# Performance work log

Measured on AMD Instinct MI355X. Metric: run time of the kernel, lower is better.

## Reference

```python
import jax, jax.numpy as jnp
import numpy as np

B = 2
SEQ = 384            # args.seq_len (per-stock sub-sequence length)
N_AUX = 4            # len(args.aux_tickers)
S = SEQ * N_AUX + 1  # global separator token + tiled sub-sequences
D_MODEL = 512
NHEAD = 8
HEAD_DIM = 64
ROPE = 32            # qk_rope_dim
KV_C = 256
Q_C = 384
D_FF = 1536
H2 = NHEAD * 2       # differential attention sub-heads
DH = HEAD_DIM // 2
RH = ROPE // 2
EPS = 1.1920929e-07  # torch RMSNorm default eps (fp32 machine eps)
SCALING = 1.0 / ((HEAD_DIM + ROPE) // 2)
LAMBDA_INIT = 0.8 - 0.6 * float(np.exp(-0.3 * 0))  # depth=0 -> 0.2


def rmsnorm(x, w, eps=EPS):
    return x * jax.lax.rsqrt(jnp.mean(jnp.square(x), -1, keepdims=True) + eps) * w


def apply_rope(xs, cos, sin):
    # xs: [B, N_AUX, SEQ, H2, RH]; cos/sin: [SEQ, RH//2]
    xr = xs[..., 0::2]
    xi = xs[..., 1::2]
    c = cos[None, None, :, None, :]
    s = sin[None, None, :, None, :]
    yr = xr * c - xi * s
    yi = xr * s + xi * c
    return jnp.stack([yr, yi], axis=-1).reshape(xs.shape)


def _build_mask():
    causal = np.triu(np.ones((SEQ, SEQ), np.bool_), 1)
    tiled = np.tile(causal, (N_AUX, N_AUX))
    m = np.ones((S, S), np.bool_)
    m[:, 0] = False          # everyone attends to global separator
    m[1:, 1:] = tiled
    return jnp.asarray(m)[None, None]  # [1,1,S,S], True = masked


MASK = _build_mask()


def setup_inputs() -> dict:
    key = jax.random.key(0)
    ks = jax.random.split(key, 16)

    def w(k, shape, std=0.02):
        return jax.random.normal(k, shape, jnp.float32) * std

    x = jax.random.normal(ks[0], (B, S, D_MODEL), jnp.float32)
    # rope table: complex [SEQ, ROPE//4] stored as (cos, sin)
    pairs = ROPE // 4
    inv = 1.0 / (10000.0 ** (np.arange(pairs, dtype=np.float64) / pairs))
    ang = np.outer(np.arange(SEQ), inv)
    freqs = jnp.asarray(np.stack([np.cos(ang), np.sin(ang)], -1), jnp.float32)
    return {
        'x': x,
        'freqs': freqs,
        'W_kv_down': w(ks[1], (D_MODEL, KV_C + ROPE)),
        'W_q_down': w(ks[2], (D_MODEL, Q_C)),
        'W_kv_up': w(ks[3], (KV_C, NHEAD * HEAD_DIM * 2)),
        'W_q_up': w(ks[4], (Q_C, NHEAD * (HEAD_DIM + ROPE))),
        'kv_norm_w': jnp.ones((KV_C,), jnp.float32),
        'q_norm_w': jnp.ones((Q_C,), jnp.float32),
        'W_o': w(ks[5], (NHEAD * HEAD_DIM, D_MODEL)),
        'lambda_q1': w(ks[6], (DH,), 0.1),
        'lambda_k1': w(ks[7], (DH,), 0.1),
        'lambda_q2': w(ks[8], (DH,), 0.1),
        'lambda_k2': w(ks[9], (DH,), 0.1),
        'head_norm_w': jnp.ones((HEAD_DIM,), jnp.float32),
        'norm1_w': jnp.ones((D_MODEL,), jnp.float32),
        'norm2_w': jnp.ones((D_MODEL,), jnp.float32),
        'W_ff_in': w(ks[10], (D_MODEL, 2 * D_FF)),
        'W_ff_out': w(ks[11], (D_FF, D_MODEL)),
    }


def reference(x, freqs, W_kv_down, W_q_down, W_kv_up, W_q_up, kv_norm_w, q_norm_w,
              W_o, lambda_q1, lambda_k1, lambda_q2, lambda_k2, head_norm_w,
              norm1_w, norm2_w, W_ff_in, W_ff_out):
    cos, sin = freqs[..., 0], freqs[..., 1]
    # ---- attention block (pre-norm) ----
    h = rmsnorm(x, norm1_w)
    ckv_full = h @ W_kv_down                               # [B,S,KV_C+ROPE]
    c_kv, k_rope = ckv_full[..., :KV_C], ckv_full[..., KV_C:]
    kv = (rmsnorm(c_kv, kv_norm_w) @ W_kv_up).reshape(B, S, NHEAD, 2 * HEAD_DIM)
    k, v = kv[..., :HEAD_DIM], kv[..., HEAD_DIM:]
    k = k.reshape(B, S, H2, DH)
    qf = (rmsnorm(h @ W_q_down, q_norm_w) @ W_q_up).reshape(B, S, NHEAD, HEAD_DIM + ROPE)
    q, q_rope = qf[..., :HEAD_DIM], qf[..., HEAD_DIM:]
    q = q.reshape(B, S, H2, DH)
    k_rope = jnp.broadcast_to(k_rope[:, :, None, :], (B, S, NHEAD, ROPE)).reshape(B, S, H2, RH)
    q_rope = q_rope.reshape(B, S, H2, RH)
    # split off global separator token, rope per sub-sequence
    q_sep, q_rot = q_rope[:, :1], q_rope[:, 1:].reshape(B, N_AUX, SEQ, H2, RH)
    k_sep, k_rot = k_rope[:, :1], k_rope[:, 1:].reshape(B, N_AUX, SEQ, H2, RH)
    q_rot = apply_rope(q_rot, cos, sin).reshape(B, S - 1, H2, RH)
    k_rot = apply_rope(k_rot, cos, sin).reshape(B, S - 1, H2, RH)
    q_rope = jnp.concatenate([q_sep, q_rot], axis=1)
    k_rope = jnp.concatenate([k_sep, k_rot], axis=1)
    qh = jnp.concatenate([q, q_rope], -1).transpose(0, 2, 1, 3)  # [B,H2,S,DH+RH]
    kh = jnp.concatenate([k, k_rope], -1).transpose(0, 2, 1, 3)
    a = jnp.einsum('bhqd,bhkd->bhqk', qh, kh) * SCALING
    abs_a = jnp.where(MASK, -1e9, jnp.abs(a))
    p = jnp.sign(a) * jax.nn.softmax(abs_a, axis=-1)
    lam = (jnp.exp(jnp.sum(lambda_q1 * lambda_k1)) -
           jnp.exp(jnp.sum(lambda_q2 * lambda_k2)) + LAMBDA_INIT)
    p = p.reshape(B, NHEAD, 2, S, S)
    G = jnp.mean(p[:, :, 0], axis=-1, keepdims=True)
    att = p[:, :, 0] - lam * p[:, :, 1] + G * lam
    att = jnp.where(MASK, 0.0, att)
    o = jnp.einsum('bhqk,bkhd->bqhd', att, v)              # [B,S,NHEAD,HEAD_DIM]
    o = rmsnorm(o, head_norm_w, 1e-5).reshape(B, S, NHEAD * HEAD_DIM)
    x = x + o @ W_o
    # ---- SwiGLU FFN ----
    h2 = rmsnorm(x, norm2_w)
    uv = h2 @ W_ff_in
    u, g = uv[..., :D_FF], uv[..., D_FF:]
    return x + (u * jax.nn.silu(g)) @ W_ff_out
```

## Files before the change

### kernel.cpp

```cpp
#include <hip/hip_runtime.h>

#define NB 2
#define SEQN 384
#define NS 1537
#define NS_PAD 1600
#define NH 8
#define H2N 16
#define NM (NB*NS)
#define DFF 1536
#define EPS1 1.1920929e-07f
#define SCAL (1.0f/48.0f)
#define SC2 (SCAL * 1.4426950408889634f)

#define SWZ(row, col) ((((row) << 6)) + ((col) ^ (((row) & 7) << 3)))

typedef __bf16 bf16x8 __attribute__((ext_vector_type(8)));
typedef _Float16 f16x8 __attribute__((ext_vector_type(8)));
typedef float f32x4 __attribute__((ext_vector_type(4)));

__device__ __forceinline__ unsigned short f2bf(float f) {
    unsigned int u = __builtin_bit_cast(unsigned int, f);
    u += 0x7FFFu + ((u >> 16) & 1u);
    return (unsigned short)(u >> 16);
}
__device__ __forceinline__ float bf2f(unsigned short h) {
    unsigned int u = ((unsigned int)h) << 16;
    return __builtin_bit_cast(float, u);
}

struct TD { const float* w; unsigned short* hi; unsigned short* lo; int K; int N; int perm; };
struct TD7 { TD d[7]; int tend[7]; };

__global__ __launch_bounds__(256) void transpose_all(TD7 a) {
    __shared__ float tile[32][33];
    int t = blockIdx.x;
    int i = 0;
    while (t >= a.tend[i]) i++;
    int base = (i == 0) ? 0 : a.tend[i - 1];
    int lt = t - base;
    const float* w = a.d[i].w;
    unsigned short* hi = a.d[i].hi;
    unsigned short* lo = a.d[i].lo;
    int K = a.d[i].K, N = a.d[i].N, perm = a.d[i].perm;
    int Nh = N >> 1;
    int kt = (K + 31) / 32;
    int k0 = (lt % kt) * 32, n0 = (lt / kt) * 32;
    int tx = threadIdx.x & 31, ty4 = (threadIdx.x >> 5) * 4;
    for (int q = 0; q < 4; q++) {
        int k = k0 + ty4 + q, n = n0 + tx;
        tile[ty4 + q][tx] = (k < K && n < N) ? w[(size_t)k * N + n] : 0.f;
    }
    __syncthreads();
    for (int q = 0; q < 4; q++) {
        int n = n0 + ty4 + q, k = k0 + tx;
        if (n < N && k < K) {
            float v = tile[tx][ty4 + q];
            unsigned short hb = f2bf(v);
            int n_out = perm ? ((n < Nh) ? 2 * n : 2 * (n - Nh) + 1) : n;
            size_t o = (size_t)n_out * K + k;
            hi[o] = hb;
            if (lo) lo[o] = f2bf(v - bf2f(hb));
        }
    }
}

__global__ __launch_bounds__(256) void rmsnorm_k(const float* __restrict__ in,
    const float* __restrict__ w, unsigned short* __restrict__ hi, unsigned short* __restrict__ lo,
    int in_stride, int C, float eps) {
    int row = blockIdx.x;
    const float* x = in + (size_t)row * in_stride;
    float ss = 0.f;
    for (int j = threadIdx.x; j < C; j += 256) { float v = x[j]; ss += v * v; }
    for (int o = 1; o < 64; o <<= 1) ss += __shfl_xor(ss, o);
    __shared__ float red[4];
    if ((threadIdx.x & 63) == 0) red[threadIdx.x >> 6] = ss;
    __syncthreads();
    ss = red[0] + red[1] + red[2] + red[3];
    float rs = rsqrtf(ss / (float)C + eps);
    for (int j = threadIdx.x; j < C; j += 256) {
        float y = x[j] * rs * w[j];
        unsigned short hb = f2bf(y);
        hi[(size_t)row * C + j] = hb;
        if (lo) lo[(size_t)row * C + j] = f2bf(y - bf2f(hb));
    }
}

__global__ __launch_bounds__(256) void rmsnorm_dual(const float* __restrict__ cq,
    const float* __restrict__ wA, const float* __restrict__ wB,
    unsigned short* __restrict__ ah, unsigned short* __restrict__ al,
    unsigned short* __restrict__ bh_, unsigned short* __restrict__ bl_) {
    int row = blockIdx.x, tid = threadIdx.x;
    const float* xx = cq + (size_t)row * 672;
    __shared__ float red[4];
    float v = xx[tid & 255];
    float ss = v * v;
    for (int o = 1; o < 64; o <<= 1) ss += __shfl_xor(ss, o);
    if ((tid & 63) == 0) red[tid >> 6] = ss;
    __syncthreads();
    float tot = red[0] + red[1] + red[2] + red[3];
    float rs = rsqrtf(tot / 256.f + EPS1);
    float y = v * rs * wA[tid];
    unsigned short hb = f2bf(y);
    ah[(size_t)row * 256 + tid] = hb;
    al[(size_t)row * 256 + tid] = f2bf(y - bf2f(hb));
    __syncthreads();
    float v0 = xx[288 + tid];
    float v1 = (tid < 128) ? xx[288 + 256 + tid] : 0.f;
    float ss2 = v0 * v0 + v1 * v1;
    for (int o = 1; o < 64; o <<= 1) ss2 += __shfl_xor(ss2, o);
    if ((tid & 63) == 0) red[tid >> 6] = ss2;
    __syncthreads();
    tot = red[0] + red[1] + red[2] + red[3];
    rs = rsqrtf(tot / 384.f + EPS1);
    float yb = v0 * rs * wB[tid];
    hb = f2bf(yb);
    bh_[(size_t)row * 384 + tid] = hb;
    bl_[(size_t)row * 384 + tid] = f2bf(yb - bf2f(hb));
    if (tid < 128) {
        float yc = v1 * rs * wB[256 + tid];
        unsigned short hc = f2bf(yc);
        bh_[(size_t)row * 384 + 256 + tid] = hc;
        bl_[(size_t)row * 384 + 256 + tid] = f2bf(yc - bf2f(hc));
    }
}

__global__ __launch_bounds__(256) void gemm_single(const unsigned short* __restrict__ A,
    const unsigned short* __restrict__ Bt, float* __restrict__ C_, const float* __restrict__ res,
    int M, int N, int K) {
    __shared__ unsigned short As[128 * 64];
    __shared__ unsigned short Bs[64 * 64];
    int m0 = blockIdx.x * 128, n0 = blockIdx.y * 64;
    int tid = threadIdx.x;
    int lane = tid & 63, wid = tid >> 6;
    int wr = wid >> 1, wc = wid & 1;
    int r = lane & 15, g = lane >> 4;
    int lrow = tid >> 3, lk = (tid & 7) * 8;
    f32x4 acc[4][2] = {};
    bool aok[4]; size_t aoff[4];
    #pragma unroll
    for (int p = 0; p < 4; p++) {
        int ar = m0 + p * 32 + lrow;
        aok[p] = ar < M;
        aoff[p] = (size_t)ar * K + lk;
    }
    bool bok[2]; size_t boff[2];
    #pragma unroll
    for (int p = 0; p < 2; p++) {
        int br = n0 + p * 32 + lrow;
        bok[p] = br < N;
        boff[p] = (size_t)br * K + lk;
    }
    for (int k0 = 0; k0 < K; k0 += 64) {
        uint4 av[4], bv[2];
        #pragma unroll
        for (int p = 0; p < 4; p++) av[p] = aok[p] ? *(const uint4*)(A + aoff[p] + k0) : (uint4){0,0,0,0};
        #pragma unroll
        for (int p = 0; p < 2; p++) bv[p] = bok[p] ? *(const uint4*)(Bt + boff[p] + k0) : (uint4){0,0,0,0};
        __syncthreads();
        #pragma unroll
        for (int p = 0; p < 4; p++) *(uint4*)&As[SWZ(p * 32 + lrow, lk)] = av[p];
        #pragma unroll
        for (int p = 0; p < 2; p++) *(uint4*)&Bs[SWZ(p * 32 + lrow, lk)] = bv[p];
        __syncthreads();
        #pragma unroll
        for (int ks = 0; ks < 2; ks++) {
            bf16x8 a[4], bb[2];
            #pragma unroll
            for (int i = 0; i < 4; i++) a[i] = *(const bf16x8*)&As[SWZ(wr * 64 + i * 16 + r, ks * 32 + g * 8)];
            #pragma unroll
            for (int j = 0; j < 2; j++) bb[j] = *(const bf16x8*)&Bs[SWZ(wc * 32 + j * 16 + r, ks * 32 + g * 8)];
            #pragma unroll
            for (int i = 0; i < 4; i++)
                #pragma unroll
                for (int j = 0; j < 2; j++)
                    acc[i][j] = __builtin_amdgcn_mfma_f32_16x16x32_bf16(a[i], bb[j], acc[i][j], 0, 0, 0);
        }
    }
    #pragma unroll
    for (int i = 0; i < 4; i++)
        #pragma unroll
        for (int j = 0; j < 2; j++) {
            int col = n0 + wc * 32 + j * 16 + r;
            if (col >= N) continue;
            #pragma unroll
            for (int e = 0; e < 4; e++) {
                int row = m0 + wr * 64 + i * 16 + g * 4 + e;
                if (row >= M) continue;
                float v = acc[i][j][e];
                if (res) v += res[(size_t)row * N + col];
                C_[(size_t)row * N + col] = v;
            }
        }
}

__global__ __launch_bounds__(256) void gemm_swiglu(const unsigned short* __restrict__ A,
    const unsigned short* __restrict__ Bt, unsigned short* __restrict__ act,
    int M, int N, int K) {
    __shared__ unsigned short As[128 * 64];
    __shared__ unsigned short Bs[64 * 64];
    int m0 = blockIdx.x * 128, n0 = blockIdx.y * 64;
    int tid = threadIdx.x;
    int lane = tid & 63, wid = tid >> 6;
    int wr = wid >> 1, wc = wid & 1;
    int r = lane & 15, g = lane >> 4;
    int lrow = tid >> 3, lk = (tid & 7) * 8;
    f32x4 acc[4][2] = {};
    bool aok[4]; size_t aoff[4];
    #pragma unroll
    for (int p = 0; p < 4; p++) {
        int ar = m0 + p * 32 + lrow;
        aok[p] = ar < M;
        aoff[p] = (size_t)ar * K + lk;
    }
    bool bok[2]; size_t boff[2];
    #pragma unroll
    for (int p = 0; p < 2; p++) {
        int br = n0 + p * 32 + lrow;
        bok[p] = br < N;
        boff[p] = (size_t)br * K + lk;
    }
    for (int k0 = 0; k0 < K; k0 += 64) {
        uint4 av[4], bv[2];
        #pragma unroll
        for (int p = 0; p < 4; p++) av[p] = aok[p] ? *(const uint4*)(A + aoff[p] + k0) : (uint4){0,0,0,0};
        #pragma unroll
        for (int p = 0; p < 2; p++) bv[p] = bok[p] ? *(const uint4*)(Bt + boff[p] + k0) : (uint4){0,0,0,0};
        __syncthreads();
        #pragma unroll
        for (int p = 0; p < 4; p++) *(uint4*)&As[SWZ(p * 32 + lrow, lk)] = av[p];
        #pragma unroll
        for (int p = 0; p < 2; p++) *(uint4*)&Bs[SWZ(p * 32 + lrow, lk)] = bv[p];
        __syncthreads();
        #pragma unroll
        for (int ks = 0; ks < 2; ks++) {
            bf16x8 a[4], bb[2];
            #pragma unroll
            for (int i = 0; i < 4; i++) a[i] = *(const bf16x8*)&As[SWZ(wr * 64 + i * 16 + r, ks * 32 + g * 8)];
            #pragma unroll
            for (int j = 0; j < 2; j++) bb[j] = *(const bf16x8*)&Bs[SWZ(wc * 32 + j * 16 + r, ks * 32 + g * 8)];
            #pragma unroll
            for (int i = 0; i < 4; i++)
                #pragma unroll
                for (int j = 0; j < 2; j++)
                    acc[i][j] = __builtin_amdgcn_mfma_f32_16x16x32_bf16(a[i], bb[j], acc[i][j], 0, 0, 0);
        }
    }
    int Nh = N >> 1;
    #pragma unroll
    for (int i = 0; i < 4; i++)
        #pragma unroll
        for (int j = 0; j < 2; j++) {
            int col = n0 + wc * 32 + j * 16 + r;
            #pragma unroll
            for (int e = 0; e < 4; e++) {
                int row = m0 + wr * 64 + i * 16 + g * 4 + e;
                float v = acc[i][j][e];
                float o = __shfl_xor(v, 1);
                if (((r & 1) == 0) && row < M && col < N) {
                    float u = v, gg = o;
                    float sg = gg / (1.f + __expf(-gg));
                    act[(size_t)row * Nh + (col >> 1)] = f2bf(u * sg);
                }
            }
        }
}

__global__ __launch_bounds__(256) void gemm_x3(const unsigned short* __restrict__ Ah,
    const unsigned short* __restrict__ Al, const unsigned short* __restrict__ Bh,
    const unsigned short* __restrict__ Bl, float* __restrict__ C_, int M, int N, int K) {
    __shared__ unsigned short AsH[128 * 64], AsL[128 * 64], BsH[64 * 64], BsL[64 * 64];
    int m0 = blockIdx.x * 128, n0 = blockIdx.y * 64;
    int tid = threadIdx.x;
    int lane = tid & 63, wid = tid >> 6;
    int wr = wid >> 1, wc = wid & 1;
    int r = lane & 15, g = lane >> 4;
    int lrow = tid >> 3, lk = (tid & 7) * 8;
    f32x4 acc[4][2] = {};
    bool aok[4]; size_t aoff[4];
    #pragma unroll
    for (int p = 0; p < 4; p++) {
        int ar = m0 + p * 32 + lrow;
        aok[p] = ar < M;
        aoff[p] = (size_t)ar * K + lk;
    }
    bool bok[2]; size_t boff[2];
    #pragma unroll
    for (int p = 0; p < 2; p++) {
        int br = n0 + p * 32 + lrow;
        bok[p] = br < N;
        boff[p] = (size_t)br * K + lk;
    }
    for (int k0 = 0; k0 < K; k0 += 64) {
        uint4 avh[4], avl[4], bvh[2], bvl[2];
        #pragma unroll
        for (int p = 0; p < 4; p++) {
            avh[p] = aok[p] ? *(const uint4*)(Ah + aoff[p] + k0) : (uint4){0,0,0,0};
            avl[p] = aok[p] ? *(const uint4*)(Al + aoff[p] + k0) : (uint4){0,0,0,0};
        }
        #pragma unroll
        for (int p = 0; p < 2; p++) {
            bvh[p] = bok[p] ? *(const uint4*)(Bh + boff[p] + k0) : (uint4){0,0,0,0};
            bvl[p] = bok[p] ? *(const uint4*)(Bl + boff[p] + k0) : (uint4){0,0,0,0};
        }
        __syncthreads();
        #pragma unroll
        for (int p = 0; p < 4; p++) {
            *(uint4*)&AsH[SWZ(p * 32 + lrow, lk)] = avh[p];
            *(uint4*)&AsL[SWZ(p * 32 + lrow, lk)] = avl[p];
        }
        #pragma unroll
        for (int p = 0; p < 2; p++) {
            *(uint4*)&BsH[SWZ(p * 32 + lrow, lk)] = bvh[p];
            *(uint4*)&BsL[SWZ(p * 32 + lrow, lk)] = bvl[p];
        }
        __syncthreads();
        #pragma unroll
        for (int ks = 0; ks < 2; ks++) {
            bf16x8 ah[4], al[4], bh[2], bl[2];
            #pragma unroll
            for (int i = 0; i < 4; i++) {
                int ai = SWZ(wr * 64 + i * 16 + r, ks * 32 + g * 8);
                ah[i] = *(const bf16x8*)&AsH[ai];
                al[i] = *(const bf16x8*)&AsL[ai];
            }
            #pragma unroll
            for (int j = 0; j < 2; j++) {
                int bi = SWZ(wc * 32 + j * 16 + r, ks * 32 + g * 8);
                bh[j] = *(const bf16x8*)&BsH[bi];
                bl[j] = *(const bf16x8*)&BsL[bi];
            }
            #pragma unroll
            for (int i = 0; i < 4; i++)
                #pragma unroll
                for (int j = 0; j < 2; j++) {
                    acc[i][j] = __builtin_amdgcn_mfma_f32_16x16x32_bf16(al[i], bh[j], acc[i][j], 0, 0, 0);
                    acc[i][j] = __builtin_amdgcn_mfma_f32_16x16x32_bf16(ah[i], bl[j], acc[i][j], 0, 0, 0);
                    acc[i][j] = __builtin_amdgcn_mfma_f32_16x16x32_bf16(ah[i], bh[j], acc[i][j], 0, 0, 0);
                }
        }
    }
    #pragma unroll
    for (int i = 0; i < 4; i++)
        #pragma unroll
        for (int j = 0; j < 2; j++) {
            int col = n0 + wc * 32 + j * 16 + r;
            if (col >= N) continue;
            #pragma unroll
            for (int e = 0; e < 4; e++) {
                int row = m0 + wr * 64 + i * 16 + g * 4 + e;
                if (row < M) C_[(size_t)row * N + col] = acc[i][j][e];
            }
        }
}

__global__ void assemble2(const float* __restrict__ qf_, const float* __restrict__ kvf,
    const float* __restrict__ cq, const float* __restrict__ freqs,
    _Float16* __restrict__ qgh, _Float16* __restrict__ qgl,
    _Float16* __restrict__ kgh, _Float16* __restrict__ kgl) {
    size_t idx = (size_t)blockIdx.x * 256 + threadIdx.x;
    const size_t total = (size_t)NB * H2N * NS_PAD * 32;
    if (idx >= total) return;
    int j2 = (int)(idx & 31);
    size_t t = idx >> 5;
    int s = (int)(t % NS_PAD); size_t r = t / NS_PAD;
    int sub = (int)(r & 1); r >>= 1;
    int h = (int)(r & 7); int b = (int)(r >> 3);
    float2 qv = make_float2(0.f, 0.f), kv2 = make_float2(0.f, 0.f);
    if (s < NS && j2 < 24) {
        size_t bs = (size_t)b * NS + s;
        if (j2 < 16) {
            const float* qp = qf_ + bs * 768 + h * 96 + sub * 32 + j2 * 2;
            qv = make_float2(qp[0], qp[1]);
            const float* kp = kvf + bs * 1024 + h * 128 + sub * 32 + j2 * 2;
            kv2 = make_float2(kp[0], kp[1]);
        } else {
            int i = j2 - 16;
            const float* qp = qf_ + bs * 768 + h * 96 + 64 + sub * 16 + 2 * i;
            float xr = qp[0], xi = qp[1];
            const float* kp = cq + bs * 672 + 256 + sub * 16 + 2 * i;
            float yr = kp[0], yi = kp[1];
            if (s == 0) {
                qv = make_float2(xr, xi);
                kv2 = make_float2(yr, yi);
            } else {
                int pos = (s - 1) % SEQN;
                float c = freqs[pos * 16 + 2 * i], sn = freqs[pos * 16 + 2 * i + 1];
                qv = make_float2(xr * c - xi * sn, xr * sn + xi * c);
                kv2 = make_float2(yr * c - yi * sn, yr * sn + yi * c);
            }
        }
    }
    _Float16 qx = (_Float16)qv.x, qy = (_Float16)qv.y;
    _Float16 kx = (_Float16)kv2.x, ky = (_Float16)kv2.y;
    qgh[idx * 2] = qx; qgh[idx * 2 + 1] = qy;
    kgh[idx * 2] = kx; kgh[idx * 2 + 1] = ky;
    qgl[idx * 2] = (_Float16)(qv.x - (float)qx); qgl[idx * 2 + 1] = (_Float16)(qv.y - (float)qy);
    kgl[idx * 2] = (_Float16)(kv2.x - (float)kx); kgl[idx * 2 + 1] = (_Float16)(kv2.y - (float)ky);
}

__global__ __launch_bounds__(256) void vtrans(const float* __restrict__ kvf,
                                              _Float16* __restrict__ vt) {
    __shared__ float tile[64][65];
    int k0 = blockIdx.x * 64;
    int b = blockIdx.y >> 3, h = blockIdx.y & 7;
    int tid = threadIdx.x;
    int row = tid >> 2, cq_ = (tid & 3) * 16;
    for (int i = 0; i < 16; i++) {
        int key = k0 + row;
        tile[row][cq_ + i] = (key < NS)
            ? kvf[((size_t)(b * NS + key)) * 1024 + h * 128 + 64 + cq_ + i] : 0.f;
    }
    __syncthreads();
    int d = tid >> 2, kq = (tid & 3) * 16;
    for (int i = 0; i < 16; i++)
        vt[((size_t)((b * 8 + h) * 64 + d)) * NS_PAD + k0 + kq + i] = (_Float16)tile[kq + i][d];
}

__global__ __launch_bounds__(256) void prefix2_k(const float* __restrict__ kvf,
                                                 float* __restrict__ P4) {
    __shared__ float tot[4][64];
    int bh = blockIdx.x; int b = bh >> 3, h = bh & 7;
    int d = threadIdx.x & 63, ps = threadIdx.x >> 6;
    int p0 = ps * 96;
    float run = 0.f;
    for (int i = 0; i < 96; i++) {
        int p = p0 + i;
        float s = 0.f;
        #pragma unroll
        for (int c = 0; c < 4; c++)
            s += kvf[((size_t)(b * NS + 1 + c * SEQN + p)) * 1024 + h * 128 + 64 + d];
        run += s;
        P4[((size_t)bh * SEQN + p) * 64 + d] = run;
    }
    tot[ps][d] = run;
    __syncthreads();
    if (ps > 0) {
        float off = 0.f;
        for (int j = 0; j < ps; j++) off += tot[j][d];
        for (int i = 0; i < 96; i++)
            P4[((size_t)bh * SEQN + p0 + i) * 64 + d] += off;
    }
}

__global__ __launch_bounds__(256) void flash_split(
    const _Float16* __restrict__ qgh, const _Float16* __restrict__ qgl,
    const _Float16* __restrict__ kgh, const _Float16* __restrict__ kgl,
    const _Float16* __restrict__ vt,
    float* __restrict__ Opart, float* __restrict__ zpart) {
    __shared__ _Float16 Ksh[2][64 * 64];
    __shared__ _Float16 Ksl[2][64 * 64];
    __shared__ _Float16 Vt[64 * 64];
    __shared__ _Float16 Pl[4][16 * 64];
    const int tile = blockIdx.x;
    const int h = blockIdx.y & 7, split = blockIdx.y >> 3;
    const int b = blockIdx.z;
    const int bh = b * 8 + h;
    const int qs0 = tile * 64;
    const int tid = threadIdx.x;
    const int wave = tid >> 6, lane = tid & 63;
    const int r = lane & 15, g = lane >> 4;
    const int qrow = qs0 + wave * 16;
    const size_t sh0 = (size_t)(bh * 2);

    f16x8 qfh[2][2], qfl[2][2];
    #pragma unroll
    for (int sub = 0; sub < 2; sub++)
        #pragma unroll
        for (int ks = 0; ks < 2; ks++) {
            size_t off = ((sh0 + sub) * NS_PAD + qrow + r) * 64 + ks * 32 + g * 8;
            qfh[sub][ks] = *(const f16x8*)(qgh + off);
            qfl[sub][ks] = *(const f16x8*)(qgl + off);
        }

    float z0p[4] = {0.f,0.f,0.f,0.f}, g0p[4] = {0.f,0.f,0.f,0.f}, z1p[4] = {0.f,0.f,0.f,0.f};
    f32x4 O0[4], O1[4];
    #pragma unroll
    for (int e = 0; e < 4; e++) { O0[e] = (f32x4){0.f,0.f,0.f,0.f}; O1[e] = (f32x4){0.f,0.f,0.f,0.f}; }
    int qpos[4];
    #pragma unroll
    for (int e = 0; e < 4; e++) {
        int q = qrow + g * 4 + e;
        qpos[e] = (q == 0) ? -1 : (q - 1) % SEQN;
    }
    int lo = qs0 < 1 ? 1 : qs0;
    int hi = qs0 + 63 < NS - 1 ? qs0 + 63 : NS - 1;
    int maxpos = ((lo - 1) / SEQN != (hi - 1) / SEQN) ? (SEQN - 1) : (hi - 1) % SEQN;

    for (int c = 2 * split; c < 2 * split + 2; c++) {
        int nb = (c == 0) ? ((maxpos + 2 + 63) >> 6) : ((maxpos + 1 + 63) >> 6);
        int kstart = (c == 0) ? 0 : (c * SEQN + 1);
        int cbase = c * SEQN + 1;
        for (int j = 0; j < nb; j++) {
            int kbase = kstart + j * 64;
            __syncthreads();
            #pragma unroll
            for (int i = 0; i < 4; i++) {
                int chunk = i * 256 + tid;
                int arr = chunk >> 9;
                int cc = chunk & 511;
                int row = cc >> 3, c8 = (cc & 7) * 8;
                size_t goff = ((sh0 + arr) * NS_PAD + kbase + row) * 64 + c8;
                int di = SWZ(row, c8);
                *(uint4*)&Ksh[arr][di] = *(const uint4*)(kgh + goff);
                *(uint4*)&Ksl[arr][di] = *(const uint4*)(kgl + goff);
            }
            #pragma unroll
            for (int i = 0; i < 2; i++) {
                int cc = i * 256 + tid;
                int d = cc >> 3, c8 = (cc & 7) * 8;
                *(uint4*)&Vt[SWZ(d, c8)] =
                    *(const uint4*)(vt + ((size_t)(bh * 64 + d)) * NS_PAD + kbase + c8);
            }
            __syncthreads();

            f16x8 bv[4][2];
            #pragma unroll
            for (int dt = 0; dt < 4; dt++)
                #pragma unroll
                for (int ks = 0; ks < 2; ks++)
                    bv[dt][ks] = *(const f16x8*)&Vt[SWZ(dt * 16 + r, ks * 32 + g * 8)];

            bool um[4][4];
            #pragma unroll
            for (int t4 = 0; t4 < 4; t4++) {
                int kk2 = kbase + t4 * 16 + r;
                int rel = kk2 - cbase;
                #pragma unroll
                for (int e = 0; e < 4; e++)
                    um[e][t4] = (kk2 == 0) ||
                                ((unsigned)rel < (unsigned)SEQN && rel <= qpos[e]);
            }

            #pragma unroll
            for (int sub = 0; sub < 2; sub++) {
                f32x4 acc[4];
                #pragma unroll
                for (int t4 = 0; t4 < 4; t4++) acc[t4] = (f32x4){0.f,0.f,0.f,0.f};
                __builtin_amdgcn_s_setprio(1);
                #pragma unroll
                for (int t4 = 0; t4 < 4; t4++)
                    #pragma unroll
                    for (int ks = 0; ks < 2; ks++) {
                        int ki = SWZ(t4 * 16 + r, ks * 32 + g * 8);
                        f16x8 bkh = *(const f16x8*)&Ksh[sub][ki];
                        f16x8 bkl = *(const f16x8*)&Ksl[sub][ki];
                        acc[t4] = __builtin_amdgcn_mfma_f32_16x16x32_f16(qfl[sub][ks], bkh, acc[t4], 0, 0, 0);
                        acc[t4] = __builtin_amdgcn_mfma_f32_16x16x32_f16(qfh[sub][ks], bkl, acc[t4], 0, 0, 0);
                        acc[t4] = __builtin_amdgcn_mfma_f32_16x16x32_f16(qfh[sub][ks], bkh, acc[t4], 0, 0, 0);
                    }
                __builtin_amdgcn_s_setprio(0);
                #pragma unroll
                for (int e = 0; e < 4; e++) {
                    #pragma unroll
                    for (int t4 = 0; t4 < 4; t4++) {
                        float a = acc[t4][e];
                        float ef = exp2f(fabsf(a) * SC2);
                        float ev = um[e][t4] ? ef : 0.f;
                        float pvv = copysignf(ev, a);
                        if (sub == 0) { z0p[e] += ev; g0p[e] += pvv; }
                        else          { z1p[e] += ev; }
                        Pl[wave][SWZ(g * 4 + e, t4 * 16 + r)] = (_Float16)pvv;
                    }
                }
                __builtin_amdgcn_wave_barrier();
                f16x8 pa0 = *(const f16x8*)&Pl[wave][SWZ(r, g * 8)];
                f16x8 pa1 = *(const f16x8*)&Pl[wave][SWZ(r, 32 + g * 8)];
                __builtin_amdgcn_s_setprio(1);
                #pragma unroll
                for (int dt = 0; dt < 4; dt++) {
                    if (sub == 0) {
                        O0[dt] = __builtin_amdgcn_mfma_f32_16x16x32_f16(pa0, bv[dt][0], O0[dt], 0, 0, 0);
                        O0[dt] = __builtin_amdgcn_mfma_f32_16x16x32_f16(pa1, bv[dt][1], O0[dt], 0, 0, 0);
                    } else {
                        O1[dt] = __builtin_amdgcn_mfma_f32_16x16x32_f16(pa0, bv[dt][0], O1[dt], 0, 0, 0);
                        O1[dt] = __builtin_amdgcn_mfma_f32_16x16x32_f16(pa1, bv[dt][1], O1[dt], 0, 0, 0);
                    }
                }
                __builtin_amdgcn_s_setprio(0);
            }
        }
    }

    #pragma unroll
    for (int e = 0; e < 4; e++) {
        float z0 = z0p[e], g0 = g0p[e], z1 = z1p[e];
        #pragma unroll
        for (int o = 1; o < 16; o <<= 1) {
            z0 += __shfl_xor(z0, o); g0 += __shfl_xor(g0, o); z1 += __shfl_xor(z1, o);
        }
        int q = qrow + g * 4 + e;
        if (q < NS) {
            if (r == 0) {
                float* zp = zpart + (((size_t)split * 16 + bh) * NS + q) * 4;
                zp[0] = z0; zp[1] = g0; zp[2] = z1;
            }
            float* op = Opart + (((size_t)split * 16 + bh) * NS + q) * 128;
            #pragma unroll
            for (int dt = 0; dt < 4; dt++) {
                op[dt * 16 + r] = O0[dt][e];
                op[64 + dt * 16 + r] = O1[dt][e];
            }
        }
    }
}

__global__ __launch_bounds__(256) void combine_attn(const float* __restrict__ Opart,
    const float* __restrict__ zpart, const float* __restrict__ kvf,
    const float* __restrict__ P4,
    const float* __restrict__ lq1, const float* __restrict__ lk1,
    const float* __restrict__ lq2, const float* __restrict__ lk2,
    const float* __restrict__ hw, unsigned short* __restrict__ o_n) {
    __shared__ float lamS;
    if (threadIdx.x < 32) {
        float p1 = lq1[threadIdx.x] * lk1[threadIdx.x];
        float p2 = lq2[threadIdx.x] * lk2[threadIdx.x];
        for (int o = 1; o < 32; o <<= 1) { p1 += __shfl_xor(p1, o); p2 += __shfl_xor(p2, o); }
        if (threadIdx.x == 0) lamS = expf(p1) - expf(p2) + 0.2f;
    }
    __syncthreads();
    float lam = lamS;
    int b = blockIdx.z, h = blockIdx.y, bh = b * 8 + h;
    int ql = threadIdx.x >> 2, dp = threadIdx.x & 3;
    int q = blockIdx.x * 64 + ql;
    bool ok = q < NS;
    int qc = ok ? q : 0;
    size_t i0 = ((size_t)0 * 16 + bh) * NS + qc;
    size_t i1 = ((size_t)1 * 16 + bh) * NS + qc;
    const float* za = zpart + i0 * 4;
    const float* zb = zpart + i1 * 4;
    float z0 = za[0] + zb[0], g0 = za[1] + zb[1], z1 = za[2] + zb[2];
    float iz0 = 1.f / z0;
    float l1 = lam / z1;
    float Gl = lam * g0 * iz0 * (1.f / (float)NS);
    int qpos = (q == 0) ? -1 : (q - 1) % SEQN;
    const float* oa = Opart + i0 * 128 + dp * 16;
    const float* ob = Opart + i1 * 128 + dp * 16;
    float of[16]; float ss = 0.f;
    #pragma unroll
    for (int i = 0; i < 16; i++) {
        int d = dp * 16 + i;
        float O0 = oa[i] + ob[i];
        float O1 = oa[64 + i] + ob[64 + i];
        float vs = kvf[((size_t)(b * NS)) * 1024 + h * 128 + 64 + d];
        if (qpos >= 0) vs += P4[((size_t)bh * SEQN + qpos) * 64 + d];
        float o = O0 * iz0 - O1 * l1 + Gl * vs;
        of[i] = o; ss += o * o;
    }
    ss += __shfl_xor(ss, 1); ss += __shfl_xor(ss, 2);
    float rs = rsqrtf(ss / 64.f + 1e-5f);
    if (ok) {
        unsigned int pk[8];
        #pragma unroll
        for (int i = 0; i < 8; i++) {
            unsigned int a = f2bf(of[2 * i] * rs * hw[dp * 16 + 2 * i]);
            unsigned int c = f2bf(of[2 * i + 1] * rs * hw[dp * 16 + 2 * i + 1]);
            pk[i] = a | (c << 16);
        }
        unsigned short* dst = o_n + ((size_t)(b * NS + q)) * 512 + h * 64 + dp * 16;
        *(uint4*)dst = *(uint4*)&pk[0];
        *(uint4*)(dst + 8) = *(uint4*)&pk[4];
    }
}

extern "C" void kernel_launch(void* const* d_in, const int* in_sizes, int n_in,
                              void* d_out, int out_size, void* d_ws, size_t ws_size,
                              hipStream_t stream) {
    (void)in_sizes; (void)n_in; (void)out_size; (void)ws_size;
    const float* x    = (const float*)d_in[0];
    const float* freqs= (const float*)d_in[1];
    const float* Wkvd = (const float*)d_in[2];
    const float* Wqd  = (const float*)d_in[3];
    const float* Wkvu = (const float*)d_in[4];
    const float* Wqu  = (const float*)d_in[5];
    const float* kvnw = (const float*)d_in[6];
    const float* qnw  = (const float*)d_in[7];
    const float* Wo   = (const float*)d_in[8];
    const float* lq1  = (const float*)d_in[9];
    const float* lk1  = (const float*)d_in[10];
    const float* lq2  = (const float*)d_in[11];
    const float* lk2  = (const float*)d_in[12];
    const float* hnw  = (const float*)d_in[13];
    const float* n1w  = (const float*)d_in[14];
    const float* n2w  = (const float*)d_in[15];
    const float* Wffi = (const float*)d_in[16];
    const float* Wffo = (const float*)d_in[17];
    float* out = (float*)d_out;

    char* p = (char*)d_ws;
    auto alloc = [&](size_t nbytes) -> char* {
        char* r = p; p += (nbytes + 255) & ~(size_t)255; return r;
    };
    unsigned short* wcq_h  = (unsigned short*)alloc((size_t)672 * 512 * 2);
    unsigned short* wcq_l  = (unsigned short*)alloc((size_t)672 * 512 * 2);
    unsigned short* wkvu_h = (unsigned short*)alloc((size_t)256 * 1024 * 2);
    unsigned short* wkvu_l = (unsigned short*)alloc((size_t)256 * 1024 * 2);
    unsigned short* wqu_h  = (unsigned short*)alloc((size_t)384 * 768 * 2);
    unsigned short* wqu_l  = (unsigned short*)alloc((size_t)384 * 768 * 2);
    unsigned short* wo_h   = (unsigned short*)alloc((size_t)512 * 512 * 2);
    unsigned short* wffi_h = (unsigned short*)alloc((size_t)512 * 3072 * 2);
    unsigned short* wffo_h = (unsigned short*)alloc((size_t)1536 * 512 * 2);
    unsigned short* h_hi   = (unsigned short*)alloc((size_t)NM * 512 * 2);
    unsigned short* h_lo   = (unsigned short*)alloc((size_t)NM * 512 * 2);
    char* cq0 = p;
    float* cq = (float*)alloc((size_t)NM * 672 * 4);
    float* x2 = (float*)cq0;
    char* nb0_ = p;
    unsigned short* ckvn_h = (unsigned short*)alloc((size_t)NM * 256 * 2);
    unsigned short* ckvn_l = (unsigned short*)alloc((size_t)NM * 256 * 2);
    unsigned short* qdn_h  = (unsigned short*)alloc((size_t)NM * 384 * 2);
    unsigned short* qdn_l  = (unsigned short*)alloc((size_t)NM * 384 * 2);
    unsigned short* o_n    = (unsigned short*)alloc((size_t)NM * 512 * 2);
    unsigned short* h2     = (unsigned short*)alloc((size_t)NM * 512 * 2);
    unsigned short* act    = (unsigned short*)nb0_;
    float* kvf = (float*)alloc((size_t)NM * 1024 * 4);
    float* qff = (float*)alloc((size_t)NM * 768 * 4);
    _Float16* qgh = (_Float16*)alloc((size_t)NB * H2N * NS_PAD * 64 * 2);
    _Float16* qgl = (_Float16*)alloc((size_t)NB * H2N * NS_PAD * 64 * 2);
    _Float16* kgh = (_Float16*)alloc((size_t)NB * H2N * NS_PAD * 64 * 2);
    _Float16* kgl = (_Float16*)alloc((size_t)NB * H2N * NS_PAD * 64 * 2);
    _Float16* vt  = (_Float16*)alloc((size_t)NB * NH * 64 * NS_PAD * 2);
    float* P4     = (float*)alloc((size_t)NB * NH * SEQN * 64 * 4);
    float* Opart  = (float*)alloc((size_t)2 * 16 * NS * 128 * 4);
    float* zpart  = (float*)alloc((size_t)2 * 16 * NS * 4 * 4);

    int cum = 0;
    {
        TD7 a;
        const float* ws_[7] = {Wkvd, Wqd, Wkvu, Wqu, Wo, Wffi, Wffo};
        unsigned short* his[7] = {wcq_h, wcq_h + (size_t)288 * 512, wkvu_h, wqu_h, wo_h, wffi_h, wffo_h};
        unsigned short* los[7] = {wcq_l, wcq_l + (size_t)288 * 512, wkvu_l, wqu_l, nullptr, nullptr, nullptr};
        int Ks[7] = {512, 512, 256, 384, 512, 512, 1536};
        int Ns[7] = {288, 384, 1024, 768, 512, 3072, 512};
        int pm[7] = {0, 0, 0, 0, 0, 1, 0};
        for (int i = 0; i < 7; i++) {
            a.d[i] = TD{ws_[i], his[i], los[i], Ks[i], Ns[i], pm[i]};
            cum += ((Ks[i] + 31) / 32) * ((Ns[i] + 31) / 32);
            a.tend[i] = cum;
        }
        transpose_all<<<dim3(cum), 256, 0, stream>>>(a);
    }

    rmsnorm_k<<<NM, 256, 0, stream>>>(x, n1w, h_hi, h_lo, 512, 512, EPS1);

    const int GX = (NM + 127) / 128;
    gemm_x3<<<dim3(GX, (672 + 63) / 64), 256, 0, stream>>>(h_hi, h_lo, wcq_h, wcq_l, cq, NM, 672, 512);

    rmsnorm_dual<<<NM, 256, 0, stream>>>(cq, kvnw, qnw, ckvn_h, ckvn_l, qdn_h, qdn_l);

    gemm_x3<<<dim3(GX, 1024 / 64), 256, 0, stream>>>(ckvn_h, ckvn_l, wkvu_h, wkvu_l, kvf, NM, 1024, 256);
    gemm_x3<<<dim3(GX, 768 / 64), 256, 0, stream>>>(qdn_h, qdn_l, wqu_h, wqu_l, qff, NM, 768, 384);

    {
        size_t total = (size_t)NB * H2N * NS_PAD * 32;
        assemble2<<<dim3((unsigned)((total + 255) / 256)), 256, 0, stream>>>(
            qff, kvf, cq, freqs, qgh, qgl, kgh, kgl);
    }
    vtrans<<<dim3(NS_PAD / 64, NB * NH), 256, 0, stream>>>(kvf, vt);
    prefix2_k<<<dim3(NB * NH), 256, 0, stream>>>(kvf, P4);

    flash_split<<<dim3((NS + 63) / 64, 16, NB), 256, 0, stream>>>(
        qgh, qgl, kgh, kgl, vt, Opart, zpart);
    combine_attn<<<dim3((NS + 63) / 64, NH, NB), 256, 0, stream>>>(
        Opart, zpart, kvf, P4, lq1, lk1, lq2, lk2, hnw, o_n);

    gemm_single<<<dim3(GX, 512 / 64), 256, 0, stream>>>(o_n, wo_h, x2, x, NM, 512, 512);
    rmsnorm_k<<<NM, 256, 0, stream>>>(x2, n2w, h2, nullptr, 512, 512, EPS1);
    gemm_swiglu<<<dim3(GX, 3072 / 64), 256, 0, stream>>>(h2, wffi_h, act, NM, 3072, 512);
    gemm_single<<<dim3(GX, 512 / 64), 256, 0, stream>>>(act, wffo_h, out, x2, NM, 512, 1536);
}
```

Before: 295.2 us.

## Load K and V fragments directly from global memory in flash_split

```diff
diff --git a/kernel.cpp b/kernel.cpp
--- a/kernel.cpp
+++ b/kernel.cpp
@@ -447,9 +447,6 @@
     const _Float16* __restrict__ kgh, const _Float16* __restrict__ kgl,
     const _Float16* __restrict__ vt,
     float* __restrict__ Opart, float* __restrict__ zpart) {
-    __shared__ _Float16 Ksh[2][64 * 64];
-    __shared__ _Float16 Ksl[2][64 * 64];
-    __shared__ _Float16 Vt[64 * 64];
     __shared__ _Float16 Pl[4][16 * 64];
     const int tile = blockIdx.x;
     const int h = blockIdx.y & 7, split = blockIdx.y >> 3;
@@ -472,6 +469,18 @@
             qfl[sub][ks] = *(const f16x8*)(qgl + off);
         }
 
+    const _Float16* khb[2], *klb[2];
+    #pragma unroll
+    for (int sub = 0; sub < 2; sub++) {
+        size_t base = ((sh0 + sub) * NS_PAD + r) * 64 + g * 8;
+        khb[sub] = kgh + base;
+        klb[sub] = kgl + base;
+    }
+    const _Float16* vbp[4];
+    #pragma unroll
+    for (int dt = 0; dt < 4; dt++)
+        vbp[dt] = vt + (size_t)(bh * 64 + dt * 16 + r) * NS_PAD + g * 8;
+
     float z0p[4] = {0.f,0.f,0.f,0.f}, g0p[4] = {0.f,0.f,0.f,0.f}, z1p[4] = {0.f,0.f,0.f,0.f};
     f32x4 O0[4], O1[4];
     #pragma unroll
@@ -492,33 +501,13 @@
         int cbase = c * SEQN + 1;
         for (int j = 0; j < nb; j++) {
             int kbase = kstart + j * 64;
-            __syncthreads();
-            #pragma unroll
-            for (int i = 0; i < 4; i++) {
-                int chunk = i * 256 + tid;
-                int arr = chunk >> 9;
-                int cc = chunk & 511;
-                int row = cc >> 3, c8 = (cc & 7) * 8;
-                size_t goff = ((sh0 + arr) * NS_PAD + kbase + row) * 64 + c8;
-                int di = SWZ(row, c8);
-                *(uint4*)&Ksh[arr][di] = *(const uint4*)(kgh + goff);
-                *(uint4*)&Ksl[arr][di] = *(const uint4*)(kgl + goff);
-            }
-            #pragma unroll
-            for (int i = 0; i < 2; i++) {
-                int cc = i * 256 + tid;
-                int d = cc >> 3, c8 = (cc & 7) * 8;
-                *(uint4*)&Vt[SWZ(d, c8)] =
-                    *(const uint4*)(vt + ((size_t)(bh * 64 + d)) * NS_PAD + kbase + c8);
-            }
-            __syncthreads();
 
             f16x8 bv[4][2];
             #pragma unroll
             for (int dt = 0; dt < 4; dt++)
                 #pragma unroll
                 for (int ks = 0; ks < 2; ks++)
-                    bv[dt][ks] = *(const f16x8*)&Vt[SWZ(dt * 16 + r, ks * 32 + g * 8)];
+                    bv[dt][ks] = *(const f16x8*)(vbp[dt] + kbase + ks * 32);
 
             bool um[4][4];
             #pragma unroll
@@ -533,6 +522,8 @@
 
             #pragma unroll
             for (int sub = 0; sub < 2; sub++) {
+                const _Float16* kh = khb[sub] + (size_t)kbase * 64;
+                const _Float16* kl = klb[sub] + (size_t)kbase * 64;
                 f32x4 acc[4];
                 #pragma unroll
                 for (int t4 = 0; t4 < 4; t4++) acc[t4] = (f32x4){0.f,0.f,0.f,0.f};
@@ -541,9 +532,8 @@
                 for (int t4 = 0; t4 < 4; t4++)
                     #pragma unroll
                     for (int ks = 0; ks < 2; ks++) {
-                        int ki = SWZ(t4 * 16 + r, ks * 32 + g * 8);
-                        f16x8 bkh = *(const f16x8*)&Ksh[sub][ki];
-                        f16x8 bkl = *(const f16x8*)&Ksl[sub][ki];
+                        f16x8 bkh = *(const f16x8*)(kh + t4 * 16 * 64 + ks * 32);
+                        f16x8 bkl = *(const f16x8*)(kl + t4 * 16 * 64 + ks * 32);
                         acc[t4] = __builtin_amdgcn_mfma_f32_16x16x32_f16(qfl[sub][ks], bkh, acc[t4], 0, 0, 0);
                         acc[t4] = __builtin_amdgcn_mfma_f32_16x16x32_f16(qfh[sub][ks], bkl, acc[t4], 0, 0, 0);
                         acc[t4] = __builtin_amdgcn_mfma_f32_16x16x32_f16(qfh[sub][ks], bkh, acc[t4], 0, 0, 0);
```

Result: slower. 492.0 us (+66.7%).
